# Performance work log

Hardware: AMD Instinct MI355X
Metric: run time of the kernel (lower is better)

The kernel has to match this reference:

```python
import jax, jax.numpy as jnp
import numpy as np

N = 128
HID = 512
NUM_IRREPS = 7

_ISO = np.array([
    [1,0,1,0,0,0,0],
    [0,1,0,1,1,0,0],
    [1,0,1,0,0,0,0],
    [0,1,0,1,1,0,0],
    [0,1,0,1,1,0,0],
    [0,0,0,0,0,1,0],
    [0,0,0,0,0,0,1],
], dtype=np.float32)


def setup_inputs() -> dict:
    key = jax.random.key(0)
    k1, k2 = jax.random.split(key)
    x = jax.random.normal(k1, (2, N, N, HID), dtype=jnp.float32)
    # xavier_uniform with relu gain on [num_irreps, num_irreps]
    gain = float(np.sqrt(2.0))
    bound = gain * float(np.sqrt(6.0 / (NUM_IRREPS + NUM_IRREPS)))
    weight = jax.random.uniform(k2, (NUM_IRREPS, NUM_IRREPS), dtype=jnp.float32,
                                minval=-bound, maxval=bound)
    iso_matrix = jnp.asarray(_ISO)
    return {"x": x, "weight": weight, "iso_matrix": iso_matrix}


def _decompose(M):
    # M: [h, n, n] -> [7, h, n, n], isotypic components under S_n conjugation.
    n = M.shape[-1]
    eye = jnp.eye(n, dtype=M.dtype)
    off = 1.0 - eye
    d = jnp.diagonal(M, axis1=-2, axis2=-1)                 # [h, n]
    dbar = jnp.mean(d, axis=-1, keepdims=True)              # [h, 1]
    P1 = dbar[..., None] * eye                              # diag mean (trivial)
    P2 = (d - dbar)[..., None] * eye                        # diag deviation (standard)
    O = M * off                                             # off-diagonal part
    s = jnp.sum(O, axis=(-2, -1)) / (n * (n - 1))           # [h]
    P3 = s[..., None, None] * off                           # offdiag mean (trivial)
    Op = O - P3
    r = jnp.sum(Op, axis=-1)                                # row sums, [h, n]
    c = jnp.sum(Op, axis=-2)                                # col sums, [h, n]
    xr = ((n - 1) * r + c) / (n * (n - 2))
    yc = ((n - 1) * c + r) / (n * (n - 2))
    P4 = xr[..., :, None] * off                             # row standard copy
    P5 = yc[..., None, :] * off                             # col standard copy
    R = Op - P4 - P5                                        # zero diag / row / col sums
    Rt = jnp.swapaxes(R, -1, -2)
    P6 = 0.5 * (R + Rt)                                     # irrep (n-2,2)
    P7 = 0.5 * (R - Rt)                                     # irrep (n-2,1,1)
    return jnp.stack([P1, P2, P3, P4, P5, P6, P7])          # [7, h, n, n]


def reference(x, weight, iso_matrix):
    # x: [2, n, n, hidden] -> transpose(1,3): [2, hidden, n, n]
    xt = jnp.transpose(x, (0, 3, 2, 1))
    A, B = xt[0], xt[1]                                     # [h, n, n]
    params = weight * iso_matrix                            # [7, 7]
    a = _decompose(A)                                       # [7, h, n, n]
    b = _decompose(B)
    # params @ comps, then sum over output irrep axis (fused into one einsum)
    A_out = jnp.einsum('ij,jhmn->hmn', params, a)
    B_out = jnp.einsum('ij,jhmn->hmn', params, b)
    out = jnp.stack([A_out, B_out])                         # [2, h, n, n]
    return jnp.transpose(out, (0, 3, 2, 1))                 # [2, n, n, hidden]
```

## Files before the change

### kernel.cpp

```cpp
#include <hip/hip_runtime.h>
#include <math.h>

#define N 128
#define HID 512
#define NH (N * HID)
#define SNH ((size_t)N * NH)
#define NPAIRS (N * (N + 1) / 2)

#define OFF_PSR 0
#define OFF_PSC 2097152
#define OFF_DG  4194304
#define OFF_XR  4325376
#define OFF_YC  4456448
#define OFF_SV  4587520
#define OFF_DB  4588544

typedef float vf4 __attribute__((ext_vector_type(4)));
union F4 { vf4 v; float f[4]; };

__global__ __launch_bounds__(512)
void schur_tile(const float* __restrict__ x,
                float* __restrict__ PSrow, float* __restrict__ PScol,
                float* __restrict__ Dg) {
    const int bi = blockIdx.x;
    const int s  = bi >> 8;
    const int ar = (bi >> 4) & 15;
    const int br = bi & 15;
    const int tid = threadIdx.x;
    const int hg  = tid & 127;
    const int qd  = tid >> 7;
    const int hoff = hg * 4;
    const bool diag = (ar == br);

    const float* tbase = x + (size_t)s * SNH + (size_t)(ar * 8) * NH
                           + (br * 8) * HID + hoff;

    F4 colacc[8];
    #pragma unroll
    for (int b = 0; b < 8; ++b) colacc[b].v = (vf4)(0.f);

    __shared__ F4 red[4][8][128];

    #pragma unroll
    for (int ra = 0; ra < 2; ++ra) {
        const int al = qd * 2 + ra;
        const float* rp = tbase + (size_t)al * NH;
        F4 rowacc; rowacc.v = (vf4)(0.f);
        F4 dgv;    dgv.v    = (vf4)(0.f);
        #pragma unroll
        for (int b = 0; b < 8; ++b) {
            F4 v; v.v = *reinterpret_cast<const vf4*>(rp + b * HID);
            rowacc.v += v.v;
            colacc[b].v += v.v;
            if (diag && b == al) dgv = v;
        }
        const int a = ar * 8 + al;
        *reinterpret_cast<vf4*>(PSrow + (((size_t)(s * 16 + br) * 128 + a) * 512 + hoff)) = rowacc.v;
        if (diag)
            *reinterpret_cast<vf4*>(Dg + (((size_t)s * 128 + a) * 512 + hoff)) = dgv.v;
    }

    #pragma unroll
    for (int b = 0; b < 8; ++b) red[qd][b][hg] = colacc[b];
    __syncthreads();

    #pragma unroll
    for (int k = 0; k < 2; ++k) {
        const int b = qd * 2 + k;
        F4 t;
        t.v = (red[0][b][hg].v + red[1][b][hg].v) + (red[2][b][hg].v + red[3][b][hg].v);
        const int gb = br * 8 + b;
        *reinterpret_cast<vf4*>(PScol + (((size_t)(s * 16 + ar) * 128 + gb) * 512 + hoff)) = t.v;
    }
}

__global__ __launch_bounds__(512)
void schur_stats(const float* __restrict__ PSrow, const float* __restrict__ PScol,
                 const float* __restrict__ Dg,
                 float* __restrict__ Xr, float* __restrict__ Yc,
                 float* __restrict__ Sv, float* __restrict__ Db) {
    const int blk = blockIdx.x;
    const int s   = blk >> 4;
    const int hc  = blk & 15;
    const int t   = threadIdx.x;
    const int iq  = t >> 5;
    const int hl  = t & 31;
    const int h   = hc * 32 + hl;

    float sa8[8], sb8[8], d8[8];
    float T = 0.f, D = 0.f;
    #pragma unroll
    for (int k = 0; k < 8; ++k) {
        const int i = iq + k * 16;
        float sa = 0.f, sb = 0.f;
        #pragma unroll
        for (int tt = 0; tt < 16; ++tt) {
            sa += PScol[((size_t)(s * 16 + tt) * 128 + i) * 512 + h];
            sb += PSrow[((size_t)(s * 16 + tt) * 128 + i) * 512 + h];
        }
        const float d = Dg[((size_t)s * 128 + i) * 512 + h];
        sa8[k] = sa; sb8[k] = sb; d8[k] = d;
        T += sa; D += d;
    }

    __shared__ float redT[16][32];
    __shared__ float redD[16][32];
    __shared__ float shS[32];
    redT[iq][hl] = T;
    redD[iq][hl] = D;
    __syncthreads();
    if (iq == 0) {
        float Tt = 0.f, Dd = 0.f;
        #pragma unroll
        for (int q = 0; q < 16; ++q) { Tt += redT[q][hl]; Dd += redD[q][hl]; }
        const float sh   = (Tt - Dd) * (1.0f / 16256.0f);
        const float dbar = Dd * (1.0f / 128.0f);
        Sv[s * HID + h] = sh;
        Db[s * HID + h] = dbar;
        shS[hl] = sh;
    }
    __syncthreads();

    const float sh    = shS[hl];
    const float k127s = 127.0f * sh;
    const float inv   = 1.0f / 16128.0f;
    const size_t base = (size_t)s * N * HID;
    #pragma unroll
    for (int k = 0; k < 8; ++k) {
        const int i = iq + k * 16;
        const float d = d8[k];
        const float r = sa8[k] - d - k127s;
        const float c = sb8[k] - d - k127s;
        Xr[base + (size_t)i * HID + h] = (127.0f * r + c) * inv;
        Yc[base + (size_t)i * HID + h] = (127.0f * c + r) * inv;
    }
}

__global__ __launch_bounds__(256)
void schur_out(const float* __restrict__ x, const float* __restrict__ w,
               const float* __restrict__ iso,
               const float* __restrict__ Xr, const float* __restrict__ Yc,
               const float* __restrict__ Sv, const float* __restrict__ Db,
               float* __restrict__ out) {
    const int t  = threadIdx.x;
    const int k  = t >> 7;
    const int ht = t & 127;
    const int hoff = ht * 4;

    float c[7];
    #pragma unroll
    for (int j = 0; j < 7; ++j) {
        float acc = 0.f;
        #pragma unroll
        for (int i = 0; i < 7; ++i) acc += w[i * 7 + j] * iso[i * 7 + j];
        c[j] = acc;
    }
    const float c1 = c[0], c2 = c[1], c3 = c[2], c4 = c[3], c5 = c[4];
    const float al = 0.5f * (c[5] + c[6]);
    const float be = 0.5f * (c[5] - c[6]);

    const int pg0 = blockIdx.x * 8;

    #define TRI_OFF(aa) ((aa) * N - (((aa) * ((aa) - 1)) >> 1))
    #pragma unroll
    for (int it = 0; it < 4; ++it) {
        const int pg = pg0 + it * 2 + k;
        const int s  = (pg >= NPAIRS) ? 1 : 0;
        const int p  = pg - s * NPAIRS;

        int a = (int)((257.0f - sqrtf((float)(66049 - 8 * p))) * 0.5f);
        if (a < 0) a = 0;
        if (a > N - 1) a = N - 1;
        while (a > 0 && TRI_OFF(a) > p) --a;
        while (TRI_OFF(a + 1) <= p) ++a;
        const int b = a + (p - TRI_OFF(a));

        const size_t sbase    = (size_t)s * SNH;
        const size_t statbase = (size_t)s * N * HID;

        if (a == b) {
            F4 v;  v.v  = *reinterpret_cast<const vf4*>(x + sbase + ((size_t)a * N + a) * HID + hoff);
            F4 db; db.v = *reinterpret_cast<const vf4*>(Db + (size_t)s * HID + hoff);
            F4 o;
            #pragma unroll
            for (int j = 0; j < 4; ++j)
                o.f[j] = c1 * db.f[j] + c2 * (v.f[j] - db.f[j]);
            __builtin_nontemporal_store(o.v,
                reinterpret_cast<vf4*>(out + sbase + ((size_t)a * N + a) * HID + hoff));
            continue;
        }

        F4 va;  va.v  = *reinterpret_cast<const vf4*>(x + sbase + ((size_t)a * N + b) * HID + hoff);
        F4 vb;  vb.v  = *reinterpret_cast<const vf4*>(x + sbase + ((size_t)b * N + a) * HID + hoff);
        F4 xra; xra.v = *reinterpret_cast<const vf4*>(Xr + statbase + (size_t)a * HID + hoff);
        F4 xrb; xrb.v = *reinterpret_cast<const vf4*>(Xr + statbase + (size_t)b * HID + hoff);
        F4 yca; yca.v = *reinterpret_cast<const vf4*>(Yc + statbase + (size_t)a * HID + hoff);
        F4 ycb; ycb.v = *reinterpret_cast<const vf4*>(Yc + statbase + (size_t)b * HID + hoff);
        F4 sh;  sh.v  = *reinterpret_cast<const vf4*>(Sv + (size_t)s * HID + hoff);

        F4 oab, oba;
        #pragma unroll
        for (int j = 0; j < 4; ++j) {
            const float U = va.f[j] - sh.f[j] - xrb.f[j] - yca.f[j];
            const float V = vb.f[j] - sh.f[j] - xra.f[j] - ycb.f[j];
            oab.f[j] = c3 * sh.f[j] + c4 * xrb.f[j] + c5 * yca.f[j] + al * U + be * V;
            oba.f[j] = c3 * sh.f[j] + c4 * xra.f[j] + c5 * ycb.f[j] + al * V + be * U;
        }
        __builtin_nontemporal_store(oab.v,
            reinterpret_cast<vf4*>(out + sbase + ((size_t)a * N + b) * HID + hoff));
        __builtin_nontemporal_store(oba.v,
            reinterpret_cast<vf4*>(out + sbase + ((size_t)b * N + a) * HID + hoff));
    }
}

extern "C" void kernel_launch(void* const* d_in, const int* in_sizes, int n_in,
                              void* d_out, int out_size, void* d_ws, size_t ws_size,
                              hipStream_t stream) {
    const float* x   = (const float*)d_in[0];
    const float* w   = (const float*)d_in[1];
    const float* iso = (const float*)d_in[2];
    float* out = (float*)d_out;
    float* ws  = (float*)d_ws;

    float* PSrow = ws + OFF_PSR;
    float* PScol = ws + OFF_PSC;
    float* Dg    = ws + OFF_DG;
    float* Xr    = ws + OFF_XR;
    float* Yc    = ws + OFF_YC;
    float* Sv    = ws + OFF_SV;
    float* Db    = ws + OFF_DB;

    schur_tile<<<512, 512, 0, stream>>>(x, PSrow, PScol, Dg);
    schur_stats<<<32, 512, 0, stream>>>(PSrow, PScol, Dg, Xr, Yc, Sv, Db);
    schur_out<<<(2 * NPAIRS) / 8, 256, 0, stream>>>(x, w, iso, Xr, Yc, Sv, Db, out);
}
```

Baseline: 52.13 us.

## Retile row/column partial-sum pass into 16x32 tiles with fewer partials

The first reduction pass now has each block cover 16 rows by 32 columns over a quarter of the hidden dimension, instead of 8x8 tiles over the full hidden dimension. Column sums accumulate in registers and row sums are reduced through shared memory. This cuts the partial-sum buffers from 16 slices to 8 column slices and 4 row slices, which lightens the stats kernel's reads. The diagonal is now fetched with a separate load. The cost is half as many blocks, extra barriers inside the reduction loop, and a larger workspace.

Result: faster. 45.78 us (-12.2%).

```diff
diff --git a/kernel.cpp b/kernel.cpp
--- a/kernel.cpp
+++ b/kernel.cpp
@@ -7,85 +7,93 @@
 #define SNH ((size_t)N * NH)
 #define NPAIRS (N * (N + 1) / 2)
 
-#define OFF_PSR 0
-#define OFF_PSC 2097152
-#define OFF_DG  4194304
-#define OFF_XR  4325376
-#define OFF_YC  4456448
-#define OFF_SV  4587520
-#define OFF_DB  4588544
+#define OFF_PSC 0
+#define OFF_PSR 4194304
+#define OFF_DG  4718592
+#define OFF_XR  4849664
+#define OFF_YC  4980736
+#define OFF_SV  5111808
+#define OFF_DB  5112832
 
 typedef float vf4 __attribute__((ext_vector_type(4)));
 union F4 { vf4 v; float f[4]; };
 
 __global__ __launch_bounds__(512)
-void schur_tile(const float* __restrict__ x,
-                float* __restrict__ PSrow, float* __restrict__ PScol,
-                float* __restrict__ Dg) {
+void schur_p1(const float* __restrict__ x, float* __restrict__ PScol,
+              float* __restrict__ PSrow, float* __restrict__ Dg) {
+    const int u  = blockIdx.x;
+    const int hq = u & 3;
+    const int bq = (u >> 2) & 3;
+    const int g  = (u >> 4) & 7;
+    const int s  = u >> 7;
+    const int tid = threadIdx.x;
+    const int f   = tid & 31;
+    const int bg  = tid >> 5;
+    const int b0  = bq * 32 + bg * 2;
+    const int hoff = hq * 128 + f * 4;
+
+    const float* xs   = x + (size_t)s * SNH;
+    const float* base = xs + (size_t)(g * 16) * NH + b0 * HID + hoff;
+
+    __shared__ F4 rowred[8][16][32];
+
+    F4 acc0, acc1;
+    acc0.v = (vf4)(0.f); acc1.v = (vf4)(0.f);
+
+    #pragma unroll
+    for (int c = 0; c < 2; ++c) {
+        #pragma unroll
+        for (int al = 0; al < 8; ++al) {
+            const float* p = base + (size_t)(c * 8 + al) * NH;
+            F4 v0; v0.v = *reinterpret_cast<const vf4*>(p);
+            F4 v1; v1.v = *reinterpret_cast<const vf4*>(p + HID);
+            acc0.v += v0.v;
+            acc1.v += v1.v;
+            F4 rs; rs.v = v0.v + v1.v;
+            rowred[al][bg][f] = rs;
+        }
+        __syncthreads();
+        if (tid < 256) {
+            const int ar = tid >> 5;
+            const int f2 = tid & 31;
+            F4 t; t.v = (vf4)(0.f);
+            #pragma unroll
+            for (int k = 0; k < 16; ++k) t.v += rowred[ar][k][f2].v;
+            const int a = g * 16 + c * 8 + ar;
+            *reinterpret_cast<vf4*>(PSrow +
+                ((((size_t)s * 4 + bq) * N + a) * HID + hq * 128 + f2 * 4)) = t.v;
+        }
+        __syncthreads();
+    }
+
+    *reinterpret_cast<vf4*>(PScol +
+        ((((size_t)s * 8 + g) * N + b0) * HID + hoff)) = acc0.v;
+    *reinterpret_cast<vf4*>(PScol +
+        ((((size_t)s * 8 + g) * N + b0 + 1) * HID + hoff)) = acc1.v;
+
+    if (bq == (g >> 1)) {
+        const int ar = tid >> 5;
+        const int f2 = tid & 31;
+        const int a  = g * 16 + ar;
+        const vf4 dv = *reinterpret_cast<const vf4*>(
+            xs + (size_t)a * NH + a * HID + hq * 128 + f2 * 4);
+        *reinterpret_cast<vf4*>(Dg +
+            (((size_t)s * N + a) * HID + hq * 128 + f2 * 4)) = dv;
+    }
+}
+
+__global__ __launch_bounds__(512)
+void schur_p2(const float* __restrict__ PScol, const float* __restrict__ PSrow,
+              const float* __restrict__ Dg,
+              float* __restrict__ Xr, float* __restrict__ Yc,
+              float* __restrict__ Sv, float* __restrict__ Db) {
     const int bi = blockIdx.x;
-    const int s  = bi >> 8;
-    const int ar = (bi >> 4) & 15;
-    const int br = bi & 15;
-    const int tid = threadIdx.x;
-    const int hg  = tid & 127;
-    const int qd  = tid >> 7;
-    const int hoff = hg * 4;
-    const bool diag = (ar == br);
-
-    const float* tbase = x + (size_t)s * SNH + (size_t)(ar * 8) * NH
-                           + (br * 8) * HID + hoff;
-
-    F4 colacc[8];
-    #pragma unroll
-    for (int b = 0; b < 8; ++b) colacc[b].v = (vf4)(0.f);
-
-    __shared__ F4 red[4][8][128];
-
-    #pragma unroll
-    for (int ra = 0; ra < 2; ++ra) {
-        const int al = qd * 2 + ra;
-        const float* rp = tbase + (size_t)al * NH;
-        F4 rowacc; rowacc.v = (vf4)(0.f);
-        F4 dgv;    dgv.v    = (vf4)(0.f);
-        #pragma unroll
-        for (int b = 0; b < 8; ++b) {
-            F4 v; v.v = *reinterpret_cast<const vf4*>(rp + b * HID);
-            rowacc.v += v.v;
-            colacc[b].v += v.v;
-            if (diag && b == al) dgv = v;
-        }
-        const int a = ar * 8 + al;
-        *reinterpret_cast<vf4*>(PSrow + (((size_t)(s * 16 + br) * 128 + a) * 512 + hoff)) = rowacc.v;
-        if (diag)
-            *reinterpret_cast<vf4*>(Dg + (((size_t)s * 128 + a) * 512 + hoff)) = dgv.v;
-    }
-
-    #pragma unroll
-    for (int b = 0; b < 8; ++b) red[qd][b][hg] = colacc[b];
-    __syncthreads();
-
-    #pragma unroll
-    for (int k = 0; k < 2; ++k) {
-        const int b = qd * 2 + k;
-        F4 t;
-        t.v = (red[0][b][hg].v + red[1][b][hg].v) + (red[2][b][hg].v + red[3][b][hg].v);
-        const int gb = br * 8 + b;
-        *reinterpret_cast<vf4*>(PScol + (((size_t)(s * 16 + ar) * 128 + gb) * 512 + hoff)) = t.v;
-    }
-}
-
-__global__ __launch_bounds__(512)
-void schur_stats(const float* __restrict__ PSrow, const float* __restrict__ PScol,
-                 const float* __restrict__ Dg,
-                 float* __restrict__ Xr, float* __restrict__ Yc,
-                 float* __restrict__ Sv, float* __restrict__ Db) {
-    const int blk = blockIdx.x;
-    const int s   = blk >> 4;
-    const int hc  = blk & 15;
-    const int t   = threadIdx.x;
-    const int iq  = t >> 5;
-    const int hl  = t & 31;
-    const int h   = hc * 32 + hl;
+    const int s  = bi >> 4;
+    const int hc = bi & 15;
+    const int t  = threadIdx.x;
+    const int iq = t >> 5;
+    const int hl = t & 31;
+    const int h  = hc * 32 + hl;
 
     float sa8[8], sb8[8], d8[8];
     float T = 0.f, D = 0.f;
@@ -94,11 +102,12 @@
         const int i = iq + k * 16;
         float sa = 0.f, sb = 0.f;
         #pragma unroll
-        for (int tt = 0; tt < 16; ++tt) {
-            sa += PScol[((size_t)(s * 16 + tt) * 128 + i) * 512 + h];
-            sb += PSrow[((size_t)(s * 16 + tt) * 128 + i) * 512 + h];
-        }
-        const float d = Dg[((size_t)s * 128 + i) * 512 + h];
+        for (int gg = 0; gg < 8; ++gg)
+            sa += PScol[(((size_t)s * 8 + gg) * N + i) * HID + h];
+        #pragma unroll
+        for (int qq = 0; qq < 4; ++qq)
+            sb += PSrow[(((size_t)s * 4 + qq) * N + i) * HID + h];
+        const float d = Dg[((size_t)s * N + i) * HID + h];
         sa8[k] = sa; sb8[k] = sb; d8[k] = d;
         T += sa; D += d;
     }
@@ -137,11 +146,11 @@
 }
 
 __global__ __launch_bounds__(256)
-void schur_out(const float* __restrict__ x, const float* __restrict__ w,
-               const float* __restrict__ iso,
-               const float* __restrict__ Xr, const float* __restrict__ Yc,
-               const float* __restrict__ Sv, const float* __restrict__ Db,
-               float* __restrict__ out) {
+void schur_p3(const float* __restrict__ x, const float* __restrict__ w,
+              const float* __restrict__ iso,
+              const float* __restrict__ Xr, const float* __restrict__ Yc,
+              const float* __restrict__ Sv, const float* __restrict__ Db,
+              float* __restrict__ out) {
     const int t  = threadIdx.x;
     const int k  = t >> 7;
     const int ht = t & 127;
@@ -222,15 +231,15 @@
     float* out = (float*)d_out;
     float* ws  = (float*)d_ws;
 
+    float* PScol = ws + OFF_PSC;
     float* PSrow = ws + OFF_PSR;
-    float* PScol = ws + OFF_PSC;
     float* Dg    = ws + OFF_DG;
     float* Xr    = ws + OFF_XR;
     float* Yc    = ws + OFF_YC;
     float* Sv    = ws + OFF_SV;
     float* Db    = ws + OFF_DB;
 
-    schur_tile<<<512, 512, 0, stream>>>(x, PSrow, PScol, Dg);
-    schur_stats<<<32, 512, 0, stream>>>(PSrow, PScol, Dg, Xr, Yc, Sv, Db);
-    schur_out<<<(2 * NPAIRS) / 8, 256, 0, stream>>>(x, w, iso, Xr, Yc, Sv, Db, out);
-}
+    schur_p1<<<256, 512, 0, stream>>>(x, PScol, PSrow, Dg);
+    schur_p2<<<32, 512, 0, stream>>>(PScol, PSrow, Dg, Xr, Yc, Sv, Db);
+    schur_p3<<<2064, 256, 0, stream>>>(x, w, iso, Xr, Yc, Sv, Db, out);
+}
```
